# Kernel tuning notes

Hardware: AMD Instinct MI355X
Metric: run time of the kernel (lower is better)

Reference implementation:

```python
import jax, jax.numpy as jnp
import numpy as np

N, E = 50000, 800000
IN_C, HID, HEADS, OUT_C = 128, 64, 4, 64
NEG_SLOPE = 0.2


def _gat_layer(x, src, dst, W, a_src, a_dst, b, heads, out_dim, concat):
    n = x.shape[0]
    h = (x @ W).reshape(n, heads, out_dim)                      # [N,H,D]
    s_src = jnp.einsum('nhd,hd->nh', h, a_src)                  # [N,H]
    s_dst = jnp.einsum('nhd,hd->nh', h, a_dst)
    e = jax.nn.leaky_relu(s_src[src] + s_dst[dst], NEG_SLOPE)   # [Etot,H]
    m = jax.ops.segment_max(e, dst, num_segments=n)             # per-dst max (self-loops => no empty segments)
    w = jnp.exp(e - m[dst])
    denom = jax.ops.segment_sum(w, dst, num_segments=n)
    alpha = w / denom[dst]                                      # segment softmax over incoming edges
    msg = h[src] * alpha[..., None]                             # [Etot,H,D] edge gather + weight
    out = jax.ops.segment_sum(msg, dst, num_segments=n)         # scatter-sum aggregate
    out = out.reshape(n, heads * out_dim) if concat else out.mean(axis=1)
    return out + b


def setup_inputs() -> dict:
    key = jax.random.key(0)
    ks = jax.random.split(key, 10)
    x = jax.random.normal(ks[0], (N, IN_C), dtype=jnp.float32)
    edge_index = jax.random.randint(ks[1], (2, E), 0, N, dtype=jnp.int64)
    s1 = 1.0 / np.sqrt(IN_C)
    s2 = 1.0 / np.sqrt(HID * HEADS)
    return {
        'x': x,
        'edge_index': edge_index,
        'W1': jax.random.normal(ks[2], (IN_C, HEADS * HID), dtype=jnp.float32) * s1,
        'a_src1': jax.random.normal(ks[3], (HEADS, HID), dtype=jnp.float32) * s1,
        'a_dst1': jax.random.normal(ks[4], (HEADS, HID), dtype=jnp.float32) * s1,
        'b1': jnp.zeros((HEADS * HID,), dtype=jnp.float32),
        'W2': jax.random.normal(ks[5], (HEADS * HID, OUT_C), dtype=jnp.float32) * s2,
        'a_src2': jax.random.normal(ks[6], (1, OUT_C), dtype=jnp.float32) * s2,
        'a_dst2': jax.random.normal(ks[7], (1, OUT_C), dtype=jnp.float32) * s2,
        'b2': jnp.zeros((OUT_C,), dtype=jnp.float32),
    }


def reference(x, edge_index, W1, a_src1, a_dst1, b1, W2, a_src2, a_dst2, b2):
    n = x.shape[0]
    loop = jnp.arange(n, dtype=edge_index.dtype)
    src = jnp.concatenate([edge_index[0], loop])  # PyG GATConv adds self-loops
    dst = jnp.concatenate([edge_index[1], loop])
    # dropout layers are identity in eval mode
    h = _gat_layer(x, src, dst, W1, a_src1, a_dst1, b1, HEADS, HID, concat=True)
    h = jax.nn.elu(h)
    h = _gat_layer(h, src, dst, W2, a_src2, a_dst2, b2, 1, OUT_C, concat=False)
    return jnp.min(h, axis=0)
```

## Files before the change

### kernel.cpp

```cpp
#include <hip/hip_runtime.h>
#include <math.h>

typedef unsigned short ushort_t;
typedef __attribute__((ext_vector_type(8))) _Float16 f16x8;
typedef __attribute__((ext_vector_type(4))) float f32x4;


__device__ inline unsigned fenc(float f) {
    unsigned u = __float_as_uint(f);
    return (u & 0x80000000u) ? ~u : (u | 0x80000000u);
}
__device__ inline float fdec(unsigned u) {
    return __uint_as_float((u & 0x80000000u) ? (u ^ 0x80000000u) : ~u);
}

__device__ inline float wrsum(float v) {
    #pragma unroll
    for (int m = 32; m; m >>= 1) v += __shfl_xor(v, m, 64);
    return v;
}
__device__ inline float lrelu(float x) { return x > 0.f ? x : 0.2f * x; }

__device__ inline ushort_t f2h(float f) {
    _Float16 h = (_Float16)f;
    union { _Float16 h; ushort_t u; } cv;
    cv.h = h;
    return cv.u;
}

#define FMAMIX_LO(acc, pk, w) \
    asm("v_fma_mix_f32 %0, %1, %2, %0 op_sel:[0,0,0] op_sel_hi:[1,0,0]" \
        : "+v"(acc) : "v"(pk), "v"(w))
#define FMAMIX_HI(acc, pk, w) \
    asm("v_fma_mix_f32 %0, %1, %2, %0 op_sel:[1,0,0] op_sel_hi:[1,0,0]" \
        : "+v"(acc) : "v"(pk), "v"(w))

__global__ __launch_bounds__(256) void pre_kernel(const float* __restrict__ W1,
                                                  const float* __restrict__ W2,
                                                  const float* __restrict__ a_src2,
                                                  const float* __restrict__ a_dst2,
                                                  ushort_t* __restrict__ W1s,
                                                  ushort_t* __restrict__ W2s,
                                                  float* __restrict__ va,
                                                  float* __restrict__ vb,
                                                  unsigned* __restrict__ minenc,
                                                  int* __restrict__ gtot) {
    int bid = blockIdx.x;
    int tid = threadIdx.x;
    if (bid < 128) {
        int idx = bid * 256 + tid;
        int j = idx & 7;
        int lane = (idx >> 3) & 63;
        int ct = (idx >> 9) & 15;
        int kc = (idx >> 13) & 3;
        int k = kc * 32 + (lane >> 4) * 8 + j;
        int c = ct * 16 + (lane & 15);
        W1s[idx] = f2h(W1[k * 256 + c]);
    } else if (bid < 192) {
        int idx = (bid - 128) * 256 + tid;
        int j = idx & 7;
        int lane = (idx >> 3) & 63;
        int ct = (idx >> 9) & 3;
        int kc = idx >> 11;
        int k = kc * 32 + (lane >> 4) * 8 + j;
        int c = ct * 16 + (lane & 15);
        W2s[idx] = f2h(W2[k * 64 + c]);
    } else {
        int k = tid;
        float sa = 0.f, sb = 0.f;
        #pragma unroll 8
        for (int c = 0; c < 64; c++) {
            float w = W2[k * 64 + c];
            sa += w * a_src2[c];
            sb += w * a_dst2[c];
        }
        va[k] = sa;
        vb[k] = sb;
        if (tid < 64) minenc[tid] = 0xFFFFFFFFu;
        gtot[tid] = 0;
    }
}

__global__ __launch_bounds__(256) void front_kernel(const float* __restrict__ x,
                                                    const ushort_t* __restrict__ W1s,
                                                    const float* __restrict__ a_src,
                                                    const float* __restrict__ a_dst,
                                                    ushort_t* __restrict__ h1b,
                                                    float* __restrict__ ssrc,
                                                    float* __restrict__ sdst,
                                                    const int* __restrict__ ei,
                                                    int* __restrict__ bh,
                                                    int* __restrict__ gtot,
                                                    int N, int E, int Etot,
                                                    int nb16, int NBA, int BB) {
    __shared__ float ss[16 * 257];
    __shared__ float ps[256];
    int bid = blockIdx.x;
    int tid = threadIdx.x;

    if (bid >= nb16) {
        int* h = (int*)ps;
        int blk = bid - nb16;
        h[tid] = 0;
        __syncthreads();
        int i0 = blk * 4096 + tid;
        #pragma unroll
        for (int e = 0; e < 16; e++) {
            int i = i0 + e * 256;
            if (i < Etot) {
                int d = (i < E) ? ei[E + i] : (i - E);
                atomicAdd(&h[d >> 8], 1);
            }
        }
        __syncthreads();
        if (tid < BB) {
            bh[tid * NBA + blk] = h[tid];
            atomicAdd(&gtot[tid], h[tid]);
        }
        return;
    }

    int base = bid * 16;
    {
        const float4* xv = (const float4*)(x + (size_t)base * 128);
        float4* xs4 = (float4*)ss;
        #pragma unroll
        for (int i = tid; i < 512; i += 256) {
            int row = i >> 5;
            float4 v = (base + row < N) ? xv[i] : make_float4(0.f, 0.f, 0.f, 0.f);
            xs4[row * 33 + (i & 31)] = v;
        }
    }
    __syncthreads();

    int lane = tid & 63, wv = tid >> 6;
    int m = lane & 15, q = lane >> 4;
    f16x8 afrag[4];
    #pragma unroll
    for (int kc = 0; kc < 4; kc++) {
        const float* xp = ss + m * 132 + kc * 32 + q * 8;
        float4 xa = *(const float4*)xp;
        float4 xb = *(const float4*)(xp + 4);
        f16x8 af;
        af[0] = (_Float16)xa.x; af[1] = (_Float16)xa.y;
        af[2] = (_Float16)xa.z; af[3] = (_Float16)xa.w;
        af[4] = (_Float16)xb.x; af[5] = (_Float16)xb.y;
        af[6] = (_Float16)xb.z; af[7] = (_Float16)xb.w;
        afrag[kc] = af;
    }
    __syncthreads();

    #pragma unroll
    for (int t = 0; t < 4; t++) {
        int ct = wv * 4 + t;
        f32x4 acc = {0.f, 0.f, 0.f, 0.f};
        #pragma unroll
        for (int kc = 0; kc < 4; kc++) {
            f16x8 bfrag = *(const f16x8*)(W1s + (((size_t)(kc * 16 + ct) * 64 + lane) << 3));
            acc = __builtin_amdgcn_mfma_f32_16x16x32_f16(afrag[kc], bfrag, acc, 0, 0, 0);
        }
        #pragma unroll
        for (int reg = 0; reg < 4; reg++) {
            ss[(q * 4 + reg) * 257 + ct * 16 + m] = acc[reg];
        }
    }
    __syncthreads();

    int dd = tid & 63, jj = tid >> 6;
    #pragma unroll
    for (int t2 = 0; t2 < 4; t2++) {
        int j = jj + t2 * 4;
        int n = base + j;
        if (n < N) {
            const float* row = ss + j * 257;
            unsigned p0 = (unsigned)f2h(row[dd]) | ((unsigned)f2h(row[64 + dd]) << 16);
            unsigned p1 = (unsigned)f2h(row[128 + dd]) | ((unsigned)f2h(row[192 + dd]) << 16);
            *(uint2*)(h1b + (size_t)n * 256 + dd * 4) = make_uint2(p0, p1);
        }
    }
    int j = tid & 15, hh2 = (tid >> 4) & 3, which = (tid >> 6) & 1, half = tid >> 7;
    const float* av = which ? a_dst : a_src;
    int cbase = hh2 * 64 + half * 32;
    float sum = 0.f;
    #pragma unroll
    for (int i = 0; i < 32; i++) {
        int ii = (i + 8 * hh2) & 31;
        sum += ss[j * 257 + cbase + ii] * av[cbase + ii];
    }
    ps[tid] = sum;
    __syncthreads();
    if (half == 0) {
        float tot = sum + ps[tid + 128];
        int n = base + j;
        if (n < N) (which ? sdst : ssrc)[n * 4 + hh2] = tot;
    }
}

__global__ __launch_bounds__(256) void scan2_kernel(int* __restrict__ bh,
                                                    const int* __restrict__ gtot,
                                                    int* __restrict__ bstart,
                                                    int NBA, int BB) {
    __shared__ int sm[256];
    int b = blockIdx.x, t = threadIdx.x;
    if (b < BB) {
        int v = (t < NBA) ? bh[b * NBA + t] : 0;
        sm[t] = v;
        __syncthreads();
        for (int o = 1; o < 256; o <<= 1) {
            int a = (t >= o) ? sm[t - o] : 0;
            __syncthreads();
            sm[t] += a;
            __syncthreads();
        }
        if (t < NBA) bh[b * NBA + t] = sm[t] - v;
    } else {
        int v = (t < BB) ? gtot[t] : 0;
        sm[t] = v;
        __syncthreads();
        for (int o = 1; o < 256; o <<= 1) {
            int a = (t >= o) ? sm[t - o] : 0;
            __syncthreads();
            sm[t] += a;
            __syncthreads();
        }
        if (t < BB) bstart[t] = sm[t] - v;
        if (t == BB - 1) bstart[BB] = sm[t];
    }
}

__global__ __launch_bounds__(256) void scat_kernel(const int* __restrict__ ei,
                                                   const int* __restrict__ bh,
                                                   const int* __restrict__ bstart,
                                                   int* __restrict__ srcbuf,
                                                   int E, int Etot, int NBA, int BB) {
    __shared__ int h[256];
    __shared__ int loff[256];
    __shared__ int gb[256];
    __shared__ int su[4096];
    __shared__ int sp[4096];
    int t = threadIdx.x, blk = blockIdx.x;
    h[t] = 0;
    __syncthreads();
    int i0 = blk * 4096;
    int blkcnt = min(4096, Etot - i0);

    int rb[16];
    #pragma unroll
    for (int e = 0; e < 16; e++) {
        int i = i0 + e * 256 + t;
        rb[e] = -1;
        if (i < Etot) {
            int d = (i < E) ? ei[E + i] : (i - E);
            int b = d >> 8;
            int r = atomicAdd(&h[b], 1);
            rb[e] = (b << 12) | r;
        }
    }
    __syncthreads();

    loff[t] = h[t];
    gb[t] = (t < BB) ? (bstart[t] + bh[t * NBA + blk]) : 0;
    __syncthreads();
    for (int o = 1; o < 256; o <<= 1) {
        int a = (t >= o) ? loff[t - o] : 0;
        __syncthreads();
        loff[t] += a;
        __syncthreads();
    }

    #pragma unroll
    for (int e = 0; e < 16; e++) {
        int i = i0 + e * 256 + t;
        if (i < Etot) {
            int s = (i < E) ? ei[i] : (i - E);
            int d = (i < E) ? ei[E + i] : (i - E);
            int b = rb[e] >> 12;
            int r = rb[e] & 0xFFF;
            int slot = loff[b] - h[b] + r;
            su[slot] = s | ((d & 255) << 16);
            sp[slot] = gb[b] + r;
        }
    }
    __syncthreads();

    for (int k = t; k < blkcnt; k += 256) {
        srcbuf[sp[k]] = su[k];
    }
}

__global__ __launch_bounds__(256) void csr_kernel(const int* __restrict__ bstart,
                                                  int* __restrict__ srcbuf,
                                                  int* __restrict__ rowptr, int N) {
    __shared__ int eb[8192];
    __shared__ unsigned short rr[8192];
    __shared__ int h[256];
    __shared__ int off[256];
    int b = blockIdx.x, t = threadIdx.x;
    int s0 = bstart[b];
    int cnt = bstart[b + 1] - s0;
    if (cnt > 8192) cnt = 8192;
    h[t] = 0;
    __syncthreads();
    for (int j = t; j < cnt; j += 256) {
        int u = srcbuf[s0 + j];
        eb[j] = u;
        rr[j] = (unsigned short)atomicAdd(&h[u >> 16], 1);
    }
    __syncthreads();
    off[t] = h[t];
    __syncthreads();
    for (int o = 1; o < 256; o <<= 1) {
        int a = (t >= o) ? off[t - o] : 0;
        __syncthreads();
        off[t] += a;
        __syncthreads();
    }
    int excl = off[t] - h[t];
    int d = b * 256 + t;
    if (d <= N) rowptr[d] = s0 + excl;
    __syncthreads();
    h[t] = excl;
    __syncthreads();
    for (int j = t; j < cnt; j += 256) {
        int u = eb[j];
        srcbuf[s0 + h[u >> 16] + rr[j]] = u & 0xFFFF;
    }
}

__global__ __launch_bounds__(256) void agg1_kernel(const int* __restrict__ rowptr,
                                                   const int* __restrict__ srcbuf,
                                                   const float* __restrict__ ssrc,
                                                   const float* __restrict__ sdst,
                                                   const ushort_t* __restrict__ h1b,
                                                   const float* __restrict__ b1,
                                                   const float* __restrict__ va,
                                                   const float* __restrict__ vb,
                                                   ushort_t* __restrict__ x2b,
                                                   float* __restrict__ ssrc2,
                                                   float* __restrict__ sdst2, int N) {
    __shared__ int    s_sh[4][64];
    __shared__ float4 w_sh[4][64];
    int lane = threadIdx.x & 63, w = threadIdx.x >> 6;
    int d = blockIdx.x * 4 + w;
    if (d >= N) return;
    int row = rowptr[d], end = rowptr[d + 1];
    float4 sd = *(const float4*)(sdst + d * 4);
    float l0 = 0.f, l1 = 0.f, l2 = 0.f, l3 = 0.f;
    float a0 = 0.f, a1 = 0.f, a2 = 0.f, a3 = 0.f;

    for (int base = row; base < end; base += 64) {
        int cnt = min(64, end - base);
        bool valid = lane < cnt;
        int s = valid ? srcbuf[base + lane] : 0;
        float4 ssv = *(const float4*)(ssrc + s * 4);
        float w0 = valid ? __expf(lrelu(ssv.x + sd.x)) : 0.f;
        float w1 = valid ? __expf(lrelu(ssv.y + sd.y)) : 0.f;
        float w2 = valid ? __expf(lrelu(ssv.z + sd.z)) : 0.f;
        float w3 = valid ? __expf(lrelu(ssv.w + sd.w)) : 0.f;
        l0 += wrsum(w0);  l1 += wrsum(w1);
        l2 += wrsum(w2);  l3 += wrsum(w3);
        s_sh[w][lane] = s;
        w_sh[w][lane] = make_float4(w0, w1, w2, w3);
        int cnt4 = (cnt + 3) & ~3;
        for (int j = 0; j < cnt4; j += 4) {
            int sj0 = s_sh[w][j], sj1 = s_sh[w][j + 1], sj2 = s_sh[w][j + 2], sj3 = s_sh[w][j + 3];
            float4 wj0 = w_sh[w][j], wj1 = w_sh[w][j + 1], wj2 = w_sh[w][j + 2], wj3 = w_sh[w][j + 3];
            uint2 u0 = *(const uint2*)(h1b + (size_t)sj0 * 256 + lane * 4);
            uint2 u1 = *(const uint2*)(h1b + (size_t)sj1 * 256 + lane * 4);
            uint2 u2 = *(const uint2*)(h1b + (size_t)sj2 * 256 + lane * 4);
            uint2 u3 = *(const uint2*)(h1b + (size_t)sj3 * 256 + lane * 4);
            FMAMIX_LO(a0, u0.x, wj0.x); FMAMIX_HI(a1, u0.x, wj0.y);
            FMAMIX_LO(a2, u0.y, wj0.z); FMAMIX_HI(a3, u0.y, wj0.w);
            FMAMIX_LO(a0, u1.x, wj1.x); FMAMIX_HI(a1, u1.x, wj1.y);
            FMAMIX_LO(a2, u1.y, wj1.z); FMAMIX_HI(a3, u1.y, wj1.w);
            FMAMIX_LO(a0, u2.x, wj2.x); FMAMIX_HI(a1, u2.x, wj2.y);
            FMAMIX_LO(a2, u2.y, wj2.z); FMAMIX_HI(a3, u2.y, wj2.w);
            FMAMIX_LO(a0, u3.x, wj3.x); FMAMIX_HI(a1, u3.x, wj3.y);
            FMAMIX_LO(a2, u3.y, wj3.z); FMAMIX_HI(a3, u3.y, wj3.w);
        }
    }
    float v0 = a0 / l0 + b1[lane];
    float v1 = a1 / l1 + b1[64 + lane];
    float v2 = a2 / l2 + b1[128 + lane];
    float v3 = a3 / l3 + b1[192 + lane];
    v0 = v0 > 0.f ? v0 : __expf(v0) - 1.f;
    v1 = v1 > 0.f ? v1 : __expf(v1) - 1.f;
    v2 = v2 > 0.f ? v2 : __expf(v2) - 1.f;
    v3 = v3 > 0.f ? v3 : __expf(v3) - 1.f;
    ushort_t* xp = x2b + (size_t)d * 256;
    xp[lane] = f2h(v0); xp[64 + lane] = f2h(v1);
    xp[128 + lane] = f2h(v2); xp[192 + lane] = f2h(v3);
    float sa = v0 * va[lane] + v1 * va[64 + lane] + v2 * va[128 + lane] + v3 * va[192 + lane];
    float sb = v0 * vb[lane] + v1 * vb[64 + lane] + v2 * vb[128 + lane] + v3 * vb[192 + lane];
    sa = wrsum(sa);
    sb = wrsum(sb);
    if (lane == 0) { ssrc2[d] = sa; sdst2[d] = sb; }
}

__global__ __launch_bounds__(256) void gemmz_kernel(const ushort_t* __restrict__ x2b,
                                                    const ushort_t* __restrict__ W2s,
                                                    const float* __restrict__ b2,
                                                    ushort_t* __restrict__ zh, int N) {
    int base = blockIdx.x * 32;
    int tid = threadIdx.x;
    int lane = tid & 63, wv = tid >> 6;
    int m = lane & 15, q = lane >> 4;
    int c = wv * 16 + m;
    float bc = b2[c];

    #pragma unroll
    for (int h = 0; h < 2; h++) {
        int rbase = base + h * 16;
        bool rowok = (rbase + m) < N;
        const ushort_t* xrow = x2b + (size_t)(rbase + m) * 256;
        f32x4 acc = {0.f, 0.f, 0.f, 0.f};
        #pragma unroll
        for (int kc = 0; kc < 8; kc++) {
            f16x8 af = {0, 0, 0, 0, 0, 0, 0, 0};
            if (rowok) af = *(const f16x8*)(xrow + kc * 32 + q * 8);
            f16x8 bf = *(const f16x8*)(W2s + (((size_t)(kc * 4 + wv) * 64 + lane) << 3));
            acc = __builtin_amdgcn_mfma_f32_16x16x32_f16(af, bf, acc, 0, 0, 0);
        }
        #pragma unroll
        for (int reg = 0; reg < 4; reg++) {
            int n = rbase + q * 4 + reg;
            if (n < N) zh[(size_t)n * 64 + c] = f2h(acc[reg] + bc);
        }
    }
}

__global__ __launch_bounds__(256) void aggz_kernel(const int* __restrict__ rowptr,
                                                   const int* __restrict__ srcbuf,
                                                   const float* __restrict__ ssrc,
                                                   const float* __restrict__ sdst,
                                                   const ushort_t* __restrict__ zh,
                                                   unsigned* __restrict__ minenc, int N) {
    __shared__ int   s_sh[4][64];
    __shared__ float w_sh[4][64];
    __shared__ float smc[4][64];
    int lane = threadIdx.x & 63, w = threadIdx.x >> 6;
    int li = lane & 31, half = lane >> 5;
    float minv0 = INFINITY, minv1 = INFINITY;

    for (int d0 = blockIdx.x * 4; d0 < N; d0 += gridDim.x * 4) {
        int d = d0 + w;
        if (d < N) {
            int row = rowptr[d], end = rowptr[d + 1];
            float sdv = sdst[d];
            float l = 0.f;
            float a0 = 0.f, a1 = 0.f;
            for (int base = row; base < end; base += 64) {
                int cnt = min(64, end - base);
                bool valid = lane < cnt;
                int s = valid ? srcbuf[base + lane] : 0;
                float wt = valid ? __expf(lrelu(ssrc[s] + sdv)) : 0.f;
                l += wrsum(wt);
                s_sh[w][lane] = s;
                w_sh[w][lane] = wt;
                int cnt4 = (cnt + 3) & ~3;
                for (int j = 0; j < cnt4; j += 4) {
                    int e0 = j + half, e1 = j + 2 + half;
                    int sj0 = s_sh[w][e0], sj1 = s_sh[w][e1];
                    float wj0 = w_sh[w][e0], wj1 = w_sh[w][e1];
                    unsigned u0 = *(const unsigned*)(zh + (size_t)sj0 * 64 + li * 2);
                    unsigned u1 = *(const unsigned*)(zh + (size_t)sj1 * 64 + li * 2);
                    FMAMIX_LO(a0, u0, wj0); FMAMIX_HI(a1, u0, wj0);
                    FMAMIX_LO(a0, u1, wj1); FMAMIX_HI(a1, u1, wj1);
                }
            }
            a0 += __shfl_xor(a0, 32, 64);
            a1 += __shfl_xor(a1, 32, 64);
            minv0 = fminf(minv0, a0 / l);
            minv1 = fminf(minv1, a1 / l);
        }
    }
    if (half == 0) {
        smc[w][2 * li] = minv0;
        smc[w][2 * li + 1] = minv1;
    }
    __syncthreads();
    if (w == 0) {
        float v = fminf(fminf(smc[0][lane], smc[1][lane]),
                        fminf(smc[2][lane], smc[3][lane]));
        atomicMin(&minenc[lane], fenc(v));
    }
}

__global__ void decode_kernel(const unsigned* __restrict__ minenc, float* __restrict__ out) {
    int d = threadIdx.x;
    if (d < 64) out[d] = fdec(minenc[d]);
}

extern "C" void kernel_launch(void* const* d_in, const int* in_sizes, int n_in,
                              void* d_out, int out_size, void* d_ws, size_t ws_size,
                              hipStream_t stream) {
    const float* x      = (const float*)d_in[0];
    const int*   ei     = (const int*)d_in[1];
    const float* W1     = (const float*)d_in[2];
    const float* a_src1 = (const float*)d_in[3];
    const float* a_dst1 = (const float*)d_in[4];
    const float* b1     = (const float*)d_in[5];
    const float* W2     = (const float*)d_in[6];
    const float* a_src2 = (const float*)d_in[7];
    const float* a_dst2 = (const float*)d_in[8];
    const float* b2     = (const float*)d_in[9];
    float* out = (float*)d_out;

    const int N = in_sizes[0] / 128;
    const int E = in_sizes[1] / 2;
    const int Etot = E + N;
    const int Epad = Etot + 64;
    const int M = N + 1;

    const int BB  = ((N - 1) >> 8) + 1;
    const int NBA = (Etot + 4095) / 4096;

    float* ws = (float*)d_ws;
    ushort_t* h1b = (ushort_t*)ws;
    ushort_t* x2b = (ushort_t*)(ws + (size_t)N * 128);
    ushort_t* zh  = (ushort_t*)(ws + (size_t)N * 256);
    ushort_t* W1s = (ushort_t*)(ws + (size_t)N * 320);
    ushort_t* W2s = (ushort_t*)(ws + (size_t)N * 320 + 16384);
    float* ssrc1  = ws + (size_t)N * 320 + 24576;
    float* sdst1  = ssrc1 + (size_t)N * 4;
    float* ssrc2  = sdst1 + (size_t)N * 4;
    float* sdst2  = ssrc2 + N;
    float* va     = sdst2 + N;
    float* vb     = va + 256;
    int*   bh     = (int*)(vb + 256);
    int*   rowptr = bh + M;
    int*   gtot   = rowptr + M;
    int*   bstart = gtot + 256;
    int*   srcbuf = bstart + 256;
    unsigned* minenc = (unsigned*)(srcbuf + Epad);

    int nb16 = (N + 15) / 16;
    int nb32 = (N + 31) / 32;
    int nb4 = (N + 3) / 4;
    int nbz = 2048;

    pre_kernel<<<193, 256, 0, stream>>>(W1, W2, a_src2, a_dst2, W1s, W2s, va, vb,
                                        minenc, gtot);
    front_kernel<<<nb16 + NBA, 256, 0, stream>>>(x, W1s, a_src1, a_dst1, h1b, ssrc1, sdst1,
                                                 ei, bh, gtot, N, E, Etot, nb16, NBA, BB);
    scan2_kernel<<<BB + 1, 256, 0, stream>>>(bh, gtot, bstart, NBA, BB);
    scat_kernel<<<NBA, 256, 0, stream>>>(ei, bh, bstart, srcbuf, E, Etot, NBA, BB);
    csr_kernel<<<BB, 256, 0, stream>>>(bstart, srcbuf, rowptr, N);

    agg1_kernel<<<nb4, 256, 0, stream>>>(rowptr, srcbuf, ssrc1, sdst1, h1b, b1,
                                         va, vb, x2b, ssrc2, sdst2, N);
    gemmz_kernel<<<nb32, 256, 0, stream>>>(x2b, W2s, b2, zh, N);
    aggz_kernel<<<nbz, 256, 0, stream>>>(rowptr, srcbuf, ssrc2, sdst2, zh, minenc, N);
    decode_kernel<<<1, 64, 0, stream>>>(minenc, out);
}
```

Measured before the change: 271.4 us.

## Widen edge-gather loads and split waves across edges in aggregation kernels

The layer-1 feature buffer is now stored in natural column order, so each lane of agg1 gathers 8 contiguous fp16 values with a 16-byte load. The two half-waves handle alternate edges, and their partial sums are merged with one shuffle at the end. aggz likewise processes four edges per step with 8-byte loads across quarter-waves. Per-chunk wave reductions of the softmax denominators are deferred to one reduction after the loop, with divides replaced by reciprocal multiplies. The intent is fewer, wider memory transactions and less shuffle overhead, at the cost of padding waste on low-degree nodes and extra cross-lane reductions.

```diff
diff --git a/kernel.cpp b/kernel.cpp
--- a/kernel.cpp
+++ b/kernel.cpp
@@ -172,9 +172,9 @@
         int j = jj + t2 * 4;
         int n = base + j;
         if (n < N) {
-            const float* row = ss + j * 257;
-            unsigned p0 = (unsigned)f2h(row[dd]) | ((unsigned)f2h(row[64 + dd]) << 16);
-            unsigned p1 = (unsigned)f2h(row[128 + dd]) | ((unsigned)f2h(row[192 + dd]) << 16);
+            const float* row = ss + j * 257 + dd * 4;
+            unsigned p0 = (unsigned)f2h(row[0]) | ((unsigned)f2h(row[1]) << 16);
+            unsigned p1 = (unsigned)f2h(row[2]) | ((unsigned)f2h(row[3]) << 16);
             *(uint2*)(h1b + (size_t)n * 256 + dd * 4) = make_uint2(p0, p1);
         }
     }
@@ -341,12 +341,15 @@
     __shared__ int    s_sh[4][64];
     __shared__ float4 w_sh[4][64];
     int lane = threadIdx.x & 63, w = threadIdx.x >> 6;
+    int li = lane & 31, half = lane >> 5;
+    int hh = li >> 3;
     int d = blockIdx.x * 4 + w;
     if (d >= N) return;
     int row = rowptr[d], end = rowptr[d + 1];
     float4 sd = *(const float4*)(sdst + d * 4);
-    float l0 = 0.f, l1 = 0.f, l2 = 0.f, l3 = 0.f;
+    float lx = 0.f, ly = 0.f, lz = 0.f, lw = 0.f;
     float a0 = 0.f, a1 = 0.f, a2 = 0.f, a3 = 0.f;
+    float a4 = 0.f, a5 = 0.f, a6 = 0.f, a7 = 0.f;
 
     for (int base = row; base < end; base += 64) {
         int cnt = min(64, end - base);
@@ -357,43 +360,64 @@
         float w1 = valid ? __expf(lrelu(ssv.y + sd.y)) : 0.f;
         float w2 = valid ? __expf(lrelu(ssv.z + sd.z)) : 0.f;
         float w3 = valid ? __expf(lrelu(ssv.w + sd.w)) : 0.f;
-        l0 += wrsum(w0);  l1 += wrsum(w1);
-        l2 += wrsum(w2);  l3 += wrsum(w3);
+        lx += w0; ly += w1; lz += w2; lw += w3;
         s_sh[w][lane] = s;
         w_sh[w][lane] = make_float4(w0, w1, w2, w3);
         int cnt4 = (cnt + 3) & ~3;
         for (int j = 0; j < cnt4; j += 4) {
-            int sj0 = s_sh[w][j], sj1 = s_sh[w][j + 1], sj2 = s_sh[w][j + 2], sj3 = s_sh[w][j + 3];
-            float4 wj0 = w_sh[w][j], wj1 = w_sh[w][j + 1], wj2 = w_sh[w][j + 2], wj3 = w_sh[w][j + 3];
-            uint2 u0 = *(const uint2*)(h1b + (size_t)sj0 * 256 + lane * 4);
-            uint2 u1 = *(const uint2*)(h1b + (size_t)sj1 * 256 + lane * 4);
-            uint2 u2 = *(const uint2*)(h1b + (size_t)sj2 * 256 + lane * 4);
-            uint2 u3 = *(const uint2*)(h1b + (size_t)sj3 * 256 + lane * 4);
-            FMAMIX_LO(a0, u0.x, wj0.x); FMAMIX_HI(a1, u0.x, wj0.y);
-            FMAMIX_LO(a2, u0.y, wj0.z); FMAMIX_HI(a3, u0.y, wj0.w);
-            FMAMIX_LO(a0, u1.x, wj1.x); FMAMIX_HI(a1, u1.x, wj1.y);
-            FMAMIX_LO(a2, u1.y, wj1.z); FMAMIX_HI(a3, u1.y, wj1.w);
-            FMAMIX_LO(a0, u2.x, wj2.x); FMAMIX_HI(a1, u2.x, wj2.y);
-            FMAMIX_LO(a2, u2.y, wj2.z); FMAMIX_HI(a3, u2.y, wj2.w);
-            FMAMIX_LO(a0, u3.x, wj3.x); FMAMIX_HI(a1, u3.x, wj3.y);
-            FMAMIX_LO(a2, u3.y, wj3.z); FMAMIX_HI(a3, u3.y, wj3.w);
-        }
-    }
-    float v0 = a0 / l0 + b1[lane];
-    float v1 = a1 / l1 + b1[64 + lane];
-    float v2 = a2 / l2 + b1[128 + lane];
-    float v3 = a3 / l3 + b1[192 + lane];
+            int ea = j + half, eb = j + 2 + half;
+            int sa_ = s_sh[w][ea], sb_ = s_sh[w][eb];
+            float wa = ((const float*)(w_sh[w] + ea))[hh];
+            float wb = ((const float*)(w_sh[w] + eb))[hh];
+            uint4 ua = *(const uint4*)(h1b + (size_t)sa_ * 256 + li * 8);
+            uint4 ub = *(const uint4*)(h1b + (size_t)sb_ * 256 + li * 8);
+            FMAMIX_LO(a0, ua.x, wa); FMAMIX_HI(a1, ua.x, wa);
+            FMAMIX_LO(a2, ua.y, wa); FMAMIX_HI(a3, ua.y, wa);
+            FMAMIX_LO(a4, ua.z, wa); FMAMIX_HI(a5, ua.z, wa);
+            FMAMIX_LO(a6, ua.w, wa); FMAMIX_HI(a7, ua.w, wa);
+            FMAMIX_LO(a0, ub.x, wb); FMAMIX_HI(a1, ub.x, wb);
+            FMAMIX_LO(a2, ub.y, wb); FMAMIX_HI(a3, ub.y, wb);
+            FMAMIX_LO(a4, ub.z, wb); FMAMIX_HI(a5, ub.z, wb);
+            FMAMIX_LO(a6, ub.w, wb); FMAMIX_HI(a7, ub.w, wb);
+        }
+    }
+    a0 += __shfl_xor(a0, 32, 64); a1 += __shfl_xor(a1, 32, 64);
+    a2 += __shfl_xor(a2, 32, 64); a3 += __shfl_xor(a3, 32, 64);
+    a4 += __shfl_xor(a4, 32, 64); a5 += __shfl_xor(a5, 32, 64);
+    a6 += __shfl_xor(a6, 32, 64); a7 += __shfl_xor(a7, 32, 64);
+    float l0 = wrsum(lx), l1 = wrsum(ly), l2 = wrsum(lz), l3 = wrsum(lw);
+    float lh = hh == 0 ? l0 : hh == 1 ? l1 : hh == 2 ? l2 : l3;
+    float rl = 1.f / lh;
+    int c8 = li * 8;
+    float4 b1a = *(const float4*)(b1 + c8);
+    float4 b1b = *(const float4*)(b1 + c8 + 4);
+    float v0 = a0 * rl + b1a.x, v1 = a1 * rl + b1a.y;
+    float v2 = a2 * rl + b1a.z, v3 = a3 * rl + b1a.w;
+    float v4 = a4 * rl + b1b.x, v5 = a5 * rl + b1b.y;
+    float v6 = a6 * rl + b1b.z, v7 = a7 * rl + b1b.w;
     v0 = v0 > 0.f ? v0 : __expf(v0) - 1.f;
     v1 = v1 > 0.f ? v1 : __expf(v1) - 1.f;
     v2 = v2 > 0.f ? v2 : __expf(v2) - 1.f;
     v3 = v3 > 0.f ? v3 : __expf(v3) - 1.f;
-    ushort_t* xp = x2b + (size_t)d * 256;
-    xp[lane] = f2h(v0); xp[64 + lane] = f2h(v1);
-    xp[128 + lane] = f2h(v2); xp[192 + lane] = f2h(v3);
-    float sa = v0 * va[lane] + v1 * va[64 + lane] + v2 * va[128 + lane] + v3 * va[192 + lane];
-    float sb = v0 * vb[lane] + v1 * vb[64 + lane] + v2 * vb[128 + lane] + v3 * vb[192 + lane];
-    sa = wrsum(sa);
-    sb = wrsum(sb);
+    v4 = v4 > 0.f ? v4 : __expf(v4) - 1.f;
+    v5 = v5 > 0.f ? v5 : __expf(v5) - 1.f;
+    v6 = v6 > 0.f ? v6 : __expf(v6) - 1.f;
+    v7 = v7 > 0.f ? v7 : __expf(v7) - 1.f;
+    if (half == 0) {
+        unsigned p0 = (unsigned)f2h(v0) | ((unsigned)f2h(v1) << 16);
+        unsigned p1 = (unsigned)f2h(v2) | ((unsigned)f2h(v3) << 16);
+        unsigned p2 = (unsigned)f2h(v4) | ((unsigned)f2h(v5) << 16);
+        unsigned p3 = (unsigned)f2h(v6) | ((unsigned)f2h(v7) << 16);
+        *(uint4*)(x2b + (size_t)d * 256 + c8) = make_uint4(p0, p1, p2, p3);
+    }
+    float4 vaa = *(const float4*)(va + c8), vab = *(const float4*)(va + c8 + 4);
+    float4 vba = *(const float4*)(vb + c8), vbb = *(const float4*)(vb + c8 + 4);
+    float sa = v0 * vaa.x + v1 * vaa.y + v2 * vaa.z + v3 * vaa.w
+             + v4 * vab.x + v5 * vab.y + v6 * vab.z + v7 * vab.w;
+    float sb = v0 * vba.x + v1 * vba.y + v2 * vba.z + v3 * vba.w
+             + v4 * vbb.x + v5 * vbb.y + v6 * vbb.z + v7 * vbb.w;
+    sa = wrsum(sa) * 0.5f;
+    sb = wrsum(sb) * 0.5f;
     if (lane == 0) { ssrc2[d] = sa; sdst2[d] = sb; }
 }
 
@@ -439,44 +463,48 @@
     __shared__ float w_sh[4][64];
     __shared__ float smc[4][64];
     int lane = threadIdx.x & 63, w = threadIdx.x >> 6;
-    int li = lane & 31, half = lane >> 5;
-    float minv0 = INFINITY, minv1 = INFINITY;
+    int li = lane & 15, q = lane >> 4;
+    float m0 = INFINITY, m1 = INFINITY, m2 = INFINITY, m3 = INFINITY;
 
     for (int d0 = blockIdx.x * 4; d0 < N; d0 += gridDim.x * 4) {
         int d = d0 + w;
         if (d < N) {
             int row = rowptr[d], end = rowptr[d + 1];
             float sdv = sdst[d];
-            float l = 0.f;
-            float a0 = 0.f, a1 = 0.f;
+            float lacc = 0.f;
+            float a0 = 0.f, a1 = 0.f, a2 = 0.f, a3 = 0.f;
             for (int base = row; base < end; base += 64) {
                 int cnt = min(64, end - base);
                 bool valid = lane < cnt;
                 int s = valid ? srcbuf[base + lane] : 0;
                 float wt = valid ? __expf(lrelu(ssrc[s] + sdv)) : 0.f;
-                l += wrsum(wt);
+                lacc += wt;
                 s_sh[w][lane] = s;
                 w_sh[w][lane] = wt;
-                int cnt4 = (cnt + 3) & ~3;
-                for (int j = 0; j < cnt4; j += 4) {
-                    int e0 = j + half, e1 = j + 2 + half;
-                    int sj0 = s_sh[w][e0], sj1 = s_sh[w][e1];
-                    float wj0 = w_sh[w][e0], wj1 = w_sh[w][e1];
-                    unsigned u0 = *(const unsigned*)(zh + (size_t)sj0 * 64 + li * 2);
-                    unsigned u1 = *(const unsigned*)(zh + (size_t)sj1 * 64 + li * 2);
-                    FMAMIX_LO(a0, u0, wj0); FMAMIX_HI(a1, u0, wj0);
-                    FMAMIX_LO(a0, u1, wj1); FMAMIX_HI(a1, u1, wj1);
+                int cnt8 = (cnt + 7) & ~7;
+                for (int j = 0; j < cnt8; j += 8) {
+                    int ea = j + q, eb = j + 4 + q;
+                    int sa_ = s_sh[w][ea], sb_ = s_sh[w][eb];
+                    float wa = w_sh[w][ea], wb = w_sh[w][eb];
+                    uint2 ua = *(const uint2*)(zh + (size_t)sa_ * 64 + li * 4);
+                    uint2 ub = *(const uint2*)(zh + (size_t)sb_ * 64 + li * 4);
+                    FMAMIX_LO(a0, ua.x, wa); FMAMIX_HI(a1, ua.x, wa);
+                    FMAMIX_LO(a2, ua.y, wa); FMAMIX_HI(a3, ua.y, wa);
+                    FMAMIX_LO(a0, ub.x, wb); FMAMIX_HI(a1, ub.x, wb);
+                    FMAMIX_LO(a2, ub.y, wb); FMAMIX_HI(a3, ub.y, wb);
                 }
             }
-            a0 += __shfl_xor(a0, 32, 64);
-            a1 += __shfl_xor(a1, 32, 64);
-            minv0 = fminf(minv0, a0 / l);
-            minv1 = fminf(minv1, a1 / l);
-        }
-    }
-    if (half == 0) {
-        smc[w][2 * li] = minv0;
-        smc[w][2 * li + 1] = minv1;
+            a0 += __shfl_xor(a0, 16, 64); a0 += __shfl_xor(a0, 32, 64);
+            a1 += __shfl_xor(a1, 16, 64); a1 += __shfl_xor(a1, 32, 64);
+            a2 += __shfl_xor(a2, 16, 64); a2 += __shfl_xor(a2, 32, 64);
+            a3 += __shfl_xor(a3, 16, 64); a3 += __shfl_xor(a3, 32, 64);
+            float rl = 1.f / wrsum(lacc);
+            m0 = fminf(m0, a0 * rl); m1 = fminf(m1, a1 * rl);
+            m2 = fminf(m2, a2 * rl); m3 = fminf(m3, a3 * rl);
+        }
+    }
+    if (q == 0) {
+        *(float4*)(&smc[w][li * 4]) = make_float4(m0, m1, m2, m3);
     }
     __syncthreads();
     if (w == 0) {
```

New measurement: 267.7 us. No clear change (-1.4%).
